# Performance work log

Hardware: AMD Instinct MI355X
Metric: run time of the kernel (lower is better)

The kernel has to match this reference:

```python
import jax, jax.numpy as jnp
import numpy as np

B, D, E, K, NC, NH = 8192, 1280, 4, 2, 20, 4
CD = D // NC      # chunk_dim = 64
HD = CD // NH     # head_dim = 16
FF = CD * 4       # ffn hidden = 256
EPS = 1e-8


def setup_inputs() -> dict:
    key = jax.random.key(0)
    ks = jax.random.split(key, 12)
    f = lambda k, sh, s=0.02: jax.random.normal(k, sh, jnp.float32) * s
    return {
        "x": jax.random.normal(ks[0], (B, D), jnp.float32),
        "gate_w1": f(ks[1], (E * 4, D)), "gate_b1": jnp.zeros((E * 4,), jnp.float32),
        "gate_w2": f(ks[2], (E, E * 4)), "gate_b2": jnp.zeros((E,), jnp.float32),
        "pos_embed": f(ks[3], (E, NC, CD)),
        "norm1_g": jnp.ones((E, CD), jnp.float32),
        "in_proj_w": f(ks[4], (E, 3 * CD, CD)), "in_proj_b": jnp.zeros((E, 3 * CD), jnp.float32),
        "out_proj_w": f(ks[5], (E, CD, CD)), "out_proj_b": jnp.zeros((E, CD), jnp.float32),
        "ls1_g": jnp.full((E, CD), 1e-4, jnp.float32),
        "norm2_g": jnp.ones((E, CD), jnp.float32),
        "ffn_w1": f(ks[6], (E, FF, CD)), "ffn_b1": jnp.zeros((E, FF), jnp.float32),
        "ffn_w2": f(ks[7], (E, CD, FF)), "ffn_b2": jnp.zeros((E, CD), jnp.float32),
        "ls2_g": jnp.full((E, CD), 1e-4, jnp.float32),
        "proj_w": f(ks[8], (E, D, D)), "proj_b": jnp.zeros((E, D), jnp.float32),
    }


def _rms(v, g):
    # torch RMSNorm in source: x / (||x||_2 * dim^-0.5 + eps) * g
    n = jnp.linalg.norm(v, axis=-1, keepdims=True) * (CD ** -0.5)
    return v / (n + EPS) * g


def _expert(x, pos, n1g, ipw, ipb, opw, opb, l1, n2g, fw1, fb1, fw2, fb2, l2, pw, pb):
    b = x.shape[0]
    xs = x.reshape(b, NC, CD) + pos            # [b, NC, CD]
    xn = _rms(xs, n1g)
    qkv = xn @ ipw.T + ipb                      # [b, NC, 3*CD]
    q, k, v = jnp.split(qkv, 3, axis=-1)
    q = q.reshape(b, NC, NH, HD).transpose(0, 2, 1, 3)
    k = k.reshape(b, NC, NH, HD).transpose(0, 2, 1, 3)
    v = v.reshape(b, NC, NH, HD).transpose(0, 2, 1, 3)
    att = jax.nn.softmax(jnp.einsum('bhqd,bhkd->bhqk', q, k) * (HD ** -0.5), axis=-1)
    o = jnp.einsum('bhqk,bhkd->bhqd', att, v).transpose(0, 2, 1, 3).reshape(b, NC, CD)
    o = o @ opw.T + opb
    xs = xs + l1 * o                            # residual + LayerScale
    h = jax.nn.relu(_rms(xs, n2g) @ fw1.T + fb1) @ fw2.T + fb2
    xs = xs + l2 * h
    return xs.reshape(b, D) @ pw.T + pb         # final proj [b, D]


def reference(x, gate_w1, gate_b1, gate_w2, gate_b2, pos_embed, norm1_g,
              in_proj_w, in_proj_b, out_proj_w, out_proj_b, ls1_g, norm2_g,
              ffn_w1, ffn_b1, ffn_w2, ffn_b2, ls2_g, proj_w, proj_b):
    logits = jnp.tanh(x @ gate_w1.T + gate_b1) @ gate_w2.T + gate_b2   # [B, E]
    scores = jax.nn.softmax(logits, axis=-1)
    tk_s, tk_i = jax.lax.top_k(scores, K)
    tk_s = tk_s / (tk_s.sum(-1, keepdims=True) + 1e-6)
    onehot = jax.nn.one_hot(tk_i, E, dtype=x.dtype)                    # [B, K, E]
    w = (onehot * tk_s[..., None]).sum(1)                              # [B, E] combine weights
    eout = jax.vmap(_expert, in_axes=(None,) + (0,) * 15)(
        x, pos_embed, norm1_g, in_proj_w, in_proj_b, out_proj_w, out_proj_b,
        ls1_g, norm2_g, ffn_w1, ffn_b1, ffn_w2, ffn_b2, ls2_g, proj_w, proj_b)  # [E, B, D]
    output = jnp.einsum('ebd,be->bd', eout, w)
    aux_loss = jnp.float32(0.0)  # eval mode
    load = onehot.sum((0, 1))    # [E]
    return output, aux_loss, load
```

## Files before the change

kernel.cpp:

```cpp
#include <hip/hip_runtime.h>
#include <hip/hip_bf16.h>
#include <math.h>

#define B_SZ 8192
#define D_SZ 1280
#define NE   4
#define NC   20
#define CD   64
#define NH   4
#define HD   16
#define FF   256

typedef __attribute__((ext_vector_type(8))) short bf16x8;
typedef __attribute__((ext_vector_type(4))) float f32x4;

#define WS_TOPI   256
#define WS_TOPW   (WS_TOPI + 2*B_SZ*4)
#define WS_IDX    (WS_TOPW + 2*B_SZ*4)
#define WS_WGT    (WS_IDX  + 2*B_SZ*4)
#define WS_ER0    (WS_WGT  + 2*B_SZ*4)
#define WS_ER1    (WS_ER0  + B_SZ*4)
#define WS_PRK    (WS_ER1  + B_SZ*4)
#define WS_BBE    (WS_PRK  + B_SZ*4)
#define WS_BBP    (WS_BBE  + 32*4*4)
#define WS_PRA    (WS_BBP  + 32*16*4)
#define WS_PRB    (WS_PRA  + (B_SZ+128)*4)
#define WS_PW1    (WS_PRB  + (B_SZ+128)*4)
#define WS_PW2    (WS_PW1  + (B_SZ+128)*4)
#define WS_PRW    (WS_PW2  + (B_SZ+128)*4)
#define WS_XSF    532480
#define XSF_ROWS  (2*B_SZ + 128)
#define WS_PWB    (WS_XSF + (size_t)XSF_ROWS * D_SZ * 2)
#define WS_IPWB   (WS_PWB  + (size_t)NE * D_SZ * D_SZ * 2)
#define WS_OPWB   (WS_IPWB + (size_t)NE * 192 * 64 * 2)
#define WS_FW1B   (WS_OPWB + (size_t)NE * 64 * 64 * 2)
#define WS_FW2B   (WS_FW1B + (size_t)NE * 256 * 64 * 2)

__global__ __launch_bounds__(256) void convert_pw(const float* __restrict__ pw,
                                                  __hip_bfloat16* __restrict__ pwb)
{
    size_t i = ((size_t)blockIdx.x * 256 + threadIdx.x) * 8;
    float4 a = *(const float4*)(pw + i);
    float4 b = *(const float4*)(pw + i + 4);
    __hip_bfloat16 h[8];
    h[0] = __float2bfloat16(a.x); h[1] = __float2bfloat16(a.y);
    h[2] = __float2bfloat16(a.z); h[3] = __float2bfloat16(a.w);
    h[4] = __float2bfloat16(b.x); h[5] = __float2bfloat16(b.y);
    h[6] = __float2bfloat16(b.z); h[7] = __float2bfloat16(b.w);
    *(uint4*)(pwb + i) = *(uint4*)h;
}

#define N_IPW (NE*192*64)
#define N_OPW (NE*64*64)
#define N_FW1 (NE*256*64)
#define N_FW2 (NE*64*256)
__global__ __launch_bounds__(256) void convert_small(
    const float* __restrict__ ipw, const float* __restrict__ opw,
    const float* __restrict__ fw1, const float* __restrict__ fw2,
    __hip_bfloat16* __restrict__ ipwb, __hip_bfloat16* __restrict__ opwb,
    __hip_bfloat16* __restrict__ fw1b, __hip_bfloat16* __restrict__ fw2b)
{
    size_t i = ((size_t)blockIdx.x * 256 + threadIdx.x) * 8;
    const float* src; __hip_bfloat16* dst; size_t off;
    if (i < N_IPW)                       { src = ipw; dst = ipwb; off = i; }
    else if (i < N_IPW + N_OPW)          { src = opw; dst = opwb; off = i - N_IPW; }
    else if (i < N_IPW + N_OPW + N_FW1)  { src = fw1; dst = fw1b; off = i - N_IPW - N_OPW; }
    else                                 { src = fw2; dst = fw2b; off = i - N_IPW - N_OPW - N_FW1; }
    float4 a = *(const float4*)(src + off);
    float4 b = *(const float4*)(src + off + 4);
    __hip_bfloat16 h[8];
    h[0] = __float2bfloat16(a.x); h[1] = __float2bfloat16(a.y);
    h[2] = __float2bfloat16(a.z); h[3] = __float2bfloat16(a.w);
    h[4] = __float2bfloat16(b.x); h[5] = __float2bfloat16(b.y);
    h[6] = __float2bfloat16(b.z); h[7] = __float2bfloat16(b.w);
    *(uint4*)(dst + off) = *(uint4*)h;
}

__global__ __launch_bounds__(64) void gate_kernel(
    const float* __restrict__ x, const float* __restrict__ gw1, const float* __restrict__ gb1,
    const float* __restrict__ gw2, const float* __restrict__ gb2,
    int* __restrict__ topi, float* __restrict__ topw)
{
    const int b = blockIdx.x;
    const int lane = threadIdx.x;
    float acc[16];
#pragma unroll
    for (int j = 0; j < 16; ++j) acc[j] = 0.f;
    const float* xr = x + (size_t)b * D_SZ;
    for (int t = 0; t < NC; ++t) {
        float xv = xr[t * 64 + lane];
#pragma unroll
        for (int j = 0; j < 16; ++j) acc[j] += xv * gw1[j * D_SZ + t * 64 + lane];
    }
#pragma unroll
    for (int j = 0; j < 16; ++j) {
        acc[j] += __shfl_xor(acc[j], 32, 64);
        acc[j] += __shfl_xor(acc[j], 16, 64);
        acc[j] += __shfl_xor(acc[j], 8, 64);
        acc[j] += __shfl_xor(acc[j], 4, 64);
        acc[j] += __shfl_xor(acc[j], 2, 64);
        acc[j] += __shfl_xor(acc[j], 1, 64);
    }
    if (lane == 0) {
        float h[16];
#pragma unroll
        for (int j = 0; j < 16; ++j) h[j] = tanhf(acc[j] + gb1[j]);
        float l[4];
#pragma unroll
        for (int e = 0; e < 4; ++e) {
            float sv = gb2[e];
#pragma unroll
            for (int j = 0; j < 16; ++j) sv += h[j] * gw2[e * 16 + j];
            l[e] = sv;
        }
        float m = fmaxf(fmaxf(l[0], l[1]), fmaxf(l[2], l[3]));
        float p[4];
        float sum = 0.f;
#pragma unroll
        for (int e = 0; e < 4; ++e) { p[e] = expf(l[e] - m); sum += p[e]; }
#pragma unroll
        for (int e = 0; e < 4; ++e) p[e] /= sum;
        int i1 = 0;
#pragma unroll
        for (int e = 1; e < 4; ++e) if (p[e] > p[i1]) i1 = e;
        int i2 = (i1 == 0) ? 1 : 0;
#pragma unroll
        for (int e = 0; e < 4; ++e) if (e != i1 && p[e] > p[i2]) i2 = e;
        float s1 = p[i1], s2 = p[i2];
        float denom = s1 + s2 + 1e-6f;
        topi[b * 2 + 0] = i1;
        topi[b * 2 + 1] = i2;
        topw[b * 2 + 0] = s1 / denom;
        topw[b * 2 + 1] = s2 / denom;
    }
}

__global__ __launch_bounds__(256) void count_kernel(
    const int* __restrict__ topi,
    int* __restrict__ cnt, int* __restrict__ pcnt,
    int* __restrict__ er0, int* __restrict__ er1, int* __restrict__ prk,
    int* __restrict__ bbe, int* __restrict__ bbp)
{
    __shared__ int he[4], hp[16];
    const int t = threadIdx.x;
    const int blk = blockIdx.x;
    const int b = blk * 256 + t;
    if (t < 4) he[t] = 0;
    if (t < 16) hp[t] = 0;
    __syncthreads();
    int e0 = topi[b * 2], e1 = topi[b * 2 + 1];
    er0[b] = atomicAdd(&he[e0], 1);
    er1[b] = atomicAdd(&he[e1], 1);
    prk[b] = atomicAdd(&hp[e0 * 4 + e1], 1);
    __syncthreads();
    if (t < 4)  bbe[blk * 4 + t]  = atomicAdd(&cnt[t], he[t]);
    if (t < 16) bbp[blk * 16 + t] = atomicAdd(&pcnt[t], hp[t]);
}

__global__ void offsets_kernel(const int* __restrict__ cnt, const int* __restrict__ pcnt,
                               int* __restrict__ offA, int* __restrict__ poff,
                               float* __restrict__ load_out)
{
    if (threadIdx.x == 0 && blockIdx.x == 0) {
        int a = 0;
#pragma unroll
        for (int e = 0; e < 4; ++e) { offA[e] = a; a += cnt[e]; }
        offA[4] = a;
        int q = 0;
#pragma unroll
        for (int p = 0; p < 16; ++p) { poff[p] = q; q += pcnt[p]; }
        poff[16] = q;
#pragma unroll
        for (int e = 0; e < 4; ++e) load_out[e] = (float)cnt[e];
    }
}

__global__ __launch_bounds__(256) void fill_kernel(
    const int* __restrict__ topi, const float* __restrict__ topw,
    const int* __restrict__ offA, const int* __restrict__ poff,
    const int* __restrict__ er0, const int* __restrict__ er1, const int* __restrict__ prk,
    const int* __restrict__ bbe, const int* __restrict__ bbp,
    int* __restrict__ idx_list, float* __restrict__ wgt_list,
    int* __restrict__ prA, int* __restrict__ prB,
    float* __restrict__ pw1, float* __restrict__ pw2, int* __restrict__ prow)
{
    const int b = blockIdx.x * 256 + threadIdx.x;
    const int blk = blockIdx.x;
    int e0 = topi[b * 2], e1 = topi[b * 2 + 1];
    float w0 = topw[b * 2], w1 = topw[b * 2 + 1];
    int slot0 = offA[e0] + bbe[blk * 4 + e0] + er0[b];
    int slot1 = offA[e1] + bbe[blk * 4 + e1] + er1[b];
    idx_list[slot0] = b; wgt_list[slot0] = w0;
    idx_list[slot1] = b; wgt_list[slot1] = w1;
    int p = e0 * 4 + e1;
    int pos = poff[p] + bbp[blk * 16 + p] + prk[b];
    prA[pos] = slot0; prB[pos] = slot1;
    pw1[pos] = w0; pw2[pos] = w1; prow[pos] = b;
}

__global__ __launch_bounds__(256) void expert_inner(
    const float* __restrict__ x, const float* __restrict__ pos,
    const float* __restrict__ n1g,
    const __hip_bfloat16* __restrict__ ipwb, const float* __restrict__ ipb,
    const __hip_bfloat16* __restrict__ opwb, const float* __restrict__ opb,
    const float* __restrict__ ls1, const float* __restrict__ n2g,
    const __hip_bfloat16* __restrict__ fw1b, const float* __restrict__ fb1,
    const __hip_bfloat16* __restrict__ fw2b, const float* __restrict__ fb2,
    const float* __restrict__ ls2,
    const int* __restrict__ offA, const int* __restrict__ idx_list,
    const float* __restrict__ wgt_list,
    __hip_bfloat16* __restrict__ xsf)
{
    __shared__ float xs[NC][66];
    __shared__ __hip_bfloat16 xnb[32][72];
    __shared__ __hip_bfloat16 qkb[32][136];
    __shared__ __hip_bfloat16 vtb[64][40];
    __shared__ __hip_bfloat16 h1b[32][264];

    const int t = threadIdx.x;
    const int w = t >> 6;
    const int lane = t & 63;
    const int l15 = lane & 15, lg = lane >> 4;
    const int s = blockIdx.x;
    const int e = (s >= offA[1]) + (s >= offA[2]) + (s >= offA[3]);
    const int b = idx_list[s];
    const float wgt = wgt_list[s];

    for (int idx = t; idx < D_SZ; idx += 256)
        xs[idx >> 6][idx & 63] = x[(size_t)b * D_SZ + idx] + pos[e * D_SZ + idx];
    __syncthreads();

    {
        float g = n1g[e * CD + lane];
#pragma unroll
        for (int ic = 0; ic < 5; ++ic) {
            int c = w * 5 + ic;
            float v = xs[c][lane];
            float ss = v * v;
            ss += __shfl_xor(ss, 32, 64); ss += __shfl_xor(ss, 16, 64);
            ss += __shfl_xor(ss, 8, 64);  ss += __shfl_xor(ss, 4, 64);
            ss += __shfl_xor(ss, 2, 64);  ss += __shfl_xor(ss, 1, 64);
            float n = sqrtf(ss) * 0.125f + 1e-8f;
            xnb[c][lane] = __float2bfloat16(v / n * g);
        }
        __hip_bfloat16 z = __float2bfloat16(0.f);
        for (int i = t; i < 12 * 64; i += 256) xnb[20 + (i >> 6)][i & 63] = z;
    }
    __syncthreads();

    {
        bf16x8 af[2][2];
#pragma unroll
        for (int mt = 0; mt < 2; ++mt)
#pragma unroll
            for (int ks = 0; ks < 2; ++ks)
                af[mt][ks] = *(const bf16x8*)&xnb[mt * 16 + l15][ks * 32 + lg * 8];
#pragma unroll
        for (int i = 0; i < 3; ++i) {
            int tn = w * 3 + i;
            int n = tn * 16 + l15;
            f32x4 acc[2] = {{0,0,0,0},{0,0,0,0}};
#pragma unroll
            for (int ks = 0; ks < 2; ++ks) {
                bf16x8 bf = *(const bf16x8*)(ipwb + ((size_t)(e * 192 + n)) * 64 + ks * 32 + lg * 8);
#pragma unroll
                for (int mt = 0; mt < 2; ++mt)
                    acc[mt] = __builtin_amdgcn_mfma_f32_16x16x32_bf16(af[mt][ks], bf, acc[mt], 0, 0, 0);
            }
            float bias = ipb[e * 192 + n];
            if (tn < 8) {
#pragma unroll
                for (int mt = 0; mt < 2; ++mt)
#pragma unroll
                    for (int r = 0; r < 4; ++r)
                        qkb[mt * 16 + lg * 4 + r][n] = __float2bfloat16(acc[mt][r] + bias);
            } else {
#pragma unroll
                for (int mt = 0; mt < 2; ++mt)
#pragma unroll
                    for (int r = 0; r < 4; ++r)
                        vtb[n - 128][mt * 16 + lg * 4 + r] = __float2bfloat16(acc[mt][r] + bias);
            }
        }
    }
    __syncthreads();

    {
        bf16x8 zf = {0,0,0,0,0,0,0,0};
        bf16x8 aq[2], bk[2];
#pragma unroll
        for (int mt = 0; mt < 2; ++mt)
            aq[mt] = (lg < 2) ? *(const bf16x8*)&qkb[mt * 16 + l15][w * 16 + lg * 8] : zf;
#pragma unroll
        for (int nt = 0; nt < 2; ++nt)
            bk[nt] = (lg < 2) ? *(const bf16x8*)&qkb[nt * 16 + l15][64 + w * 16 + lg * 8] : zf;
        f32x4 sacc[2][2];
#pragma unroll
        for (int mt = 0; mt < 2; ++mt)
#pragma unroll
            for (int nt = 0; nt < 2; ++nt)
                sacc[mt][nt] = __builtin_amdgcn_mfma_f32_16x16x32_bf16(
                    aq[mt], bk[nt], (f32x4){0,0,0,0}, 0, 0, 0);

#pragma unroll
        for (int mt = 0; mt < 2; ++mt) {
#pragma unroll
            for (int r = 0; r < 4; ++r) {
                float v0 = sacc[mt][0][r] * 0.25f;
                float v1 = (l15 < 4) ? sacc[mt][1][r] * 0.25f : -3.0e38f;
                float mx = fmaxf(v0, v1);
                mx = fmaxf(mx, __shfl_xor(mx, 1, 64));
                mx = fmaxf(mx, __shfl_xor(mx, 2, 64));
                mx = fmaxf(mx, __shfl_xor(mx, 4, 64));
                mx = fmaxf(mx, __shfl_xor(mx, 8, 64));
                float e0 = __expf(v0 - mx);
                float e1 = (l15 < 4) ? __expf(v1 - mx) : 0.f;
                float sm = e0 + e1;
                sm += __shfl_xor(sm, 1, 64);
                sm += __shfl_xor(sm, 2, 64);
                sm += __shfl_xor(sm, 4, 64);
                sm += __shfl_xor(sm, 8, 64);
                float is = 1.0f / sm;
                int qi = mt * 16 + lg * 4 + r;
                h1b[qi][w * 32 + l15]      = __float2bfloat16(e0 * is);
                h1b[qi][w * 32 + 16 + l15] = __float2bfloat16(e1 * is);
            }
        }
        bf16x8 bv = *(const bf16x8*)&vtb[w * 16 + l15][lg * 8];
#pragma unroll
        for (int mt = 0; mt < 2; ++mt) {
            bf16x8 ap = *(const bf16x8*)&h1b[mt * 16 + l15][w * 32 + lg * 8];
            f32x4 oacc = __builtin_amdgcn_mfma_f32_16x16x32_bf16(ap, bv, (f32x4){0,0,0,0}, 0, 0, 0);
#pragma unroll
            for (int r = 0; r < 4; ++r)
                xnb[mt * 16 + lg * 4 + r][w * 16 + l15] = __float2bfloat16(oacc[r]);
        }
    }
    __syncthreads();

    {
        bf16x8 af[2][2];
#pragma unroll
        for (int mt = 0; mt < 2; ++mt)
#pragma unroll
            for (int ks = 0; ks < 2; ++ks)
                af[mt][ks] = *(const bf16x8*)&xnb[mt * 16 + l15][ks * 32 + lg * 8];
        int n = w * 16 + l15;
        f32x4 acc[2] = {{0,0,0,0},{0,0,0,0}};
#pragma unroll
        for (int ks = 0; ks < 2; ++ks) {
            bf16x8 bf = *(const bf16x8*)(opwb + ((size_t)(e * 64 + n)) * 64 + ks * 32 + lg * 8);
#pragma unroll
            for (int mt = 0; mt < 2; ++mt)
                acc[mt] = __builtin_amdgcn_mfma_f32_16x16x32_bf16(af[mt][ks], bf, acc[mt], 0, 0, 0);
        }
        float l1v = ls1[e * 64 + n], ob = opb[e * 64 + n];
#pragma unroll
        for (int mt = 0; mt < 2; ++mt)
#pragma unroll
            for (int r = 0; r < 4; ++r) {
                int m = mt * 16 + lg * 4 + r;
                if (m < NC) xs[m][n] += l1v * (acc[mt][r] + ob);
            }
    }
    __syncthreads();

    {
        float g = n2g[e * CD + lane];
#pragma unroll
        for (int ic = 0; ic < 5; ++ic) {
            int c = w * 5 + ic;
            float v = xs[c][lane];
            float ss = v * v;
            ss += __shfl_xor(ss, 32, 64); ss += __shfl_xor(ss, 16, 64);
            ss += __shfl_xor(ss, 8, 64);  ss += __shfl_xor(ss, 4, 64);
            ss += __shfl_xor(ss, 2, 64);  ss += __shfl_xor(ss, 1, 64);
            float n = sqrtf(ss) * 0.125f + 1e-8f;
            xnb[c][lane] = __float2bfloat16(v / n * g);
        }
        __hip_bfloat16 z = __float2bfloat16(0.f);
        for (int i = t; i < 12 * 64; i += 256) xnb[20 + (i >> 6)][i & 63] = z;
    }
    __syncthreads();

    {
        bf16x8 af[2][2];
#pragma unroll
        for (int mt = 0; mt < 2; ++mt)
#pragma unroll
            for (int ks = 0; ks < 2; ++ks)
                af[mt][ks] = *(const bf16x8*)&xnb[mt * 16 + l15][ks * 32 + lg * 8];
#pragma unroll
        for (int i = 0; i < 4; ++i) {
            int n = (w * 4 + i) * 16 + l15;
            f32x4 acc[2] = {{0,0,0,0},{0,0,0,0}};
#pragma unroll
            for (int ks = 0; ks < 2; ++ks) {
                bf16x8 bf = *(const bf16x8*)(fw1b + ((size_t)(e * 256 + n)) * 64 + ks * 32 + lg * 8);
#pragma unroll
                for (int mt = 0; mt < 2; ++mt)
                    acc[mt] = __builtin_amdgcn_mfma_f32_16x16x32_bf16(af[mt][ks], bf, acc[mt], 0, 0, 0);
            }
            float b1 = fb1[e * 256 + n];
#pragma unroll
            for (int mt = 0; mt < 2; ++mt)
#pragma unroll
                for (int r = 0; r < 4; ++r)
                    h1b[mt * 16 + lg * 4 + r][n] = __float2bfloat16(fmaxf(acc[mt][r] + b1, 0.f));
        }
    }
    __syncthreads();

    {
        int n = w * 16 + l15;
        f32x4 acc[2] = {{0,0,0,0},{0,0,0,0}};
#pragma unroll
        for (int ks = 0; ks < 8; ++ks) {
            bf16x8 bf = *(const bf16x8*)(fw2b + ((size_t)(e * 64 + n)) * 256 + ks * 32 + lg * 8);
#pragma unroll
            for (int mt = 0; mt < 2; ++mt) {
                bf16x8 af = *(const bf16x8*)&h1b[mt * 16 + l15][ks * 32 + lg * 8];
                acc[mt] = __builtin_amdgcn_mfma_f32_16x16x32_bf16(af, bf, acc[mt], 0, 0, 0);
            }
        }
        float l2v = ls2[e * 64 + n], b2 = fb2[e * 64 + n];
#pragma unroll
        for (int mt = 0; mt < 2; ++mt)
#pragma unroll
            for (int r = 0; r < 4; ++r) {
                int m = mt * 16 + lg * 4 + r;
                if (m < NC) xs[m][n] += l2v * (acc[mt][r] + b2);
            }
    }
    __syncthreads();

    for (int idx = t; idx < D_SZ; idx += 256)
        xsf[(size_t)s * D_SZ + idx] = __float2bfloat16(wgt * xs[idx >> 6][idx & 63]);
}

#define PROWP 130

__global__ __launch_bounds__(256) void proj_pair(
    const __hip_bfloat16* __restrict__ xsf, const __hip_bfloat16* __restrict__ pwb,
    const float* __restrict__ pb, const int* __restrict__ poff,
    const int* __restrict__ prA, const int* __restrict__ prB,
    const float* __restrict__ pw1, const float* __restrict__ pw2,
    const int* __restrict__ prow, float* __restrict__ out)
{
    __shared__ short As[8][PROWP][8];
    __shared__ short Bs[8][PROWP][8];
    __shared__ int   sSlot[2][128];
    __shared__ float sW[2][128];
    __shared__ int   sRow[128];

    int mblk = blockIdx.x;
    int p = 0, base = 0, M = 0;
#pragma unroll
    for (int pp = 0; pp < 16; ++pp) {
        int b0 = poff[pp], b1 = poff[pp + 1];
        int nb = (b1 - b0 + 127) >> 7;
        if (p == pp && mblk >= nb) { mblk -= nb; p = pp + 1; }
        else if (p == pp) { base = b0; M = b1 - b0; }
    }
    if (p >= 16) return;
    const int ea = p >> 2, eb = p & 3;

    const int m0 = mblk * 128;
    const int n0 = blockIdx.y * 128;
    const int t = threadIdx.x;
    const int w = t >> 6, lane = t & 63;
    const int wm = (w & 1) * 64, wn = (w >> 1) * 64;
    const int l15 = lane & 15, lg = lane >> 4;

    if (t < 128) {
        int posn = base + m0 + t;
        int sa = prA[posn], sb = prB[posn];
        sSlot[0][t] = min(max(sa, 0), 2 * B_SZ);
        sSlot[1][t] = min(max(sb, 0), 2 * B_SZ);
        sW[0][t] = pw1[posn]; sW[1][t] = pw2[posn];
        sRow[t] = prow[posn];
    }
    __syncthreads();

    f32x4 acc[4][4];
#pragma unroll
    for (int i = 0; i < 4; ++i)
#pragma unroll
        for (int j = 0; j < 4; ++j) acc[i][j] = (f32x4){0.f, 0.f, 0.f, 0.f};

    const int arow0 = t >> 3;
    const int akb = t & 7;

#pragma unroll
    for (int ph = 0; ph < 2; ++ph) {
        const __hip_bfloat16* Bg = pwb + (size_t)(ph ? eb : ea) * D_SZ * D_SZ + (size_t)n0 * D_SZ;
        int aslot[4];
#pragma unroll
        for (int i = 0; i < 4; ++i) aslot[i] = sSlot[ph][arow0 + 32 * i];

        for (int kt = 0; kt < D_SZ; kt += 64) {
            __syncthreads();
#pragma unroll
            for (int i = 0; i < 4; ++i) {
                int row = arow0 + 32 * i;
                *(uint4*)&As[akb][row][0] =
                    *(const uint4*)(xsf + (size_t)aslot[i] * D_SZ + kt + akb * 8);
                *(uint4*)&Bs[akb][row][0] =
                    *(const uint4*)(Bg + (size_t)row * D_SZ + kt + akb * 8);
            }
            __syncthreads();
#pragma unroll
            for (int ks = 0; ks < 2; ++ks) {
                int kb = ks * 4 + lg;
                bf16x8 af[4], bfr[4];
#pragma unroll
                for (int ti = 0; ti < 4; ++ti) af[ti]  = *(const bf16x8*)&As[kb][wm + ti * 16 + l15][0];
#pragma unroll
                for (int tj = 0; tj < 4; ++tj) bfr[tj] = *(const bf16x8*)&Bs[kb][wn + tj * 16 + l15][0];
#pragma unroll
                for (int ti = 0; ti < 4; ++ti)
#pragma unroll
                    for (int tj = 0; tj < 4; ++tj)
                        acc[ti][tj] = __builtin_amdgcn_mfma_f32_16x16x32_bf16(
                            af[ti], bfr[tj], acc[ti][tj], 0, 0, 0);
            }
        }
    }

    float pbva[4], pbvb[4];
#pragma unroll
    for (int tj = 0; tj < 4; ++tj) {
        int nc = n0 + wn + tj * 16 + l15;
        pbva[tj] = pb[(size_t)ea * D_SZ + nc];
        pbvb[tj] = pb[(size_t)eb * D_SZ + nc];
    }

#pragma unroll
    for (int ti = 0; ti < 4; ++ti) {
#pragma unroll
        for (int r = 0; r < 4; ++r) {
            int m = wm + ti * 16 + lg * 4 + r;
            if (m0 + m < M) {
                float w1 = sW[0][m], w2 = sW[1][m];
                float* orow = out + (size_t)sRow[m] * D_SZ + n0 + wn + l15;
#pragma unroll
                for (int tj = 0; tj < 4; ++tj)
                    orow[tj * 16] = acc[ti][tj][r] + w1 * pbva[tj] + w2 * pbvb[tj];
            }
        }
    }
}

extern "C" void kernel_launch(void* const* d_in, const int* in_sizes, int n_in,
                              void* d_out, int out_size, void* d_ws, size_t ws_size,
                              hipStream_t stream)
{
    const float* x   = (const float*)d_in[0];
    const float* gw1 = (const float*)d_in[1];
    const float* gb1 = (const float*)d_in[2];
    const float* gw2 = (const float*)d_in[3];
    const float* gb2 = (const float*)d_in[4];
    const float* pos = (const float*)d_in[5];
    const float* n1g = (const float*)d_in[6];
    const float* ipw = (const float*)d_in[7];
    const float* ipb = (const float*)d_in[8];
    const float* opw = (const float*)d_in[9];
    const float* opb = (const float*)d_in[10];
    const float* ls1 = (const float*)d_in[11];
    const float* n2g = (const float*)d_in[12];
    const float* fw1 = (const float*)d_in[13];
    const float* fb1 = (const float*)d_in[14];
    const float* fw2 = (const float*)d_in[15];
    const float* fb2 = (const float*)d_in[16];
    const float* ls2 = (const float*)d_in[17];
    const float* pw  = (const float*)d_in[18];
    const float* pb  = (const float*)d_in[19];

    float* out = (float*)d_out;

    char* ws = (char*)d_ws;
    int*   cnt      = (int*)(ws + 0);
    int*   pcnt     = (int*)(ws + 16);
    int*   offA     = (int*)(ws + 80);
    int*   poff     = (int*)(ws + 112);
    int*   topi     = (int*)(ws + WS_TOPI);
    float* topw     = (float*)(ws + WS_TOPW);
    int*   idx_list = (int*)(ws + WS_IDX);
    float* wgt_list = (float*)(ws + WS_WGT);
    int*   er0      = (int*)(ws + WS_ER0);
    int*   er1      = (int*)(ws + WS_ER1);
    int*   prk      = (int*)(ws + WS_PRK);
    int*   bbe      = (int*)(ws + WS_BBE);
    int*   bbp      = (int*)(ws + WS_BBP);
    int*   prA      = (int*)(ws + WS_PRA);
    int*   prB      = (int*)(ws + WS_PRB);
    float* pw1      = (float*)(ws + WS_PW1);
    float* pw2      = (float*)(ws + WS_PW2);
    int*   prow     = (int*)(ws + WS_PRW);
    __hip_bfloat16* xsf  = (__hip_bfloat16*)(ws + WS_XSF);
    __hip_bfloat16* pwb  = (__hip_bfloat16*)(ws + WS_PWB);
    __hip_bfloat16* ipwb = (__hip_bfloat16*)(ws + WS_IPWB);
    __hip_bfloat16* opwb = (__hip_bfloat16*)(ws + WS_OPWB);
    __hip_bfloat16* fw1b = (__hip_bfloat16*)(ws + WS_FW1B);
    __hip_bfloat16* fw2b = (__hip_bfloat16*)(ws + WS_FW2B);

    hipMemsetAsync(d_ws, 0, 256, stream);
    hipMemsetAsync(out + (size_t)B_SZ * D_SZ, 0, 5 * sizeof(float), stream);

    float* load_out = out + (size_t)B_SZ * D_SZ + 1;

    convert_pw<<<NE * D_SZ * D_SZ / (256 * 8), 256, 0, stream>>>(pw, pwb);
    convert_small<<<(N_IPW + N_OPW + N_FW1 + N_FW2) / (256 * 8), 256, 0, stream>>>(
        ipw, opw, fw1, fw2, ipwb, opwb, fw1b, fw2b);
    gate_kernel<<<B_SZ, 64, 0, stream>>>(x, gw1, gb1, gw2, gb2, topi, topw);
    count_kernel<<<B_SZ / 256, 256, 0, stream>>>(topi, cnt, pcnt, er0, er1, prk, bbe, bbp);
    offsets_kernel<<<1, 64, 0, stream>>>(cnt, pcnt, offA, poff, load_out);
    fill_kernel<<<B_SZ / 256, 256, 0, stream>>>(topi, topw, offA, poff, er0, er1, prk,
                                                bbe, bbp, idx_list, wgt_list,
                                                prA, prB, pw1, pw2, prow);
    expert_inner<<<2 * B_SZ, 256, 0, stream>>>(x, pos, n1g, ipwb, ipb, opwb, opb, ls1,
                                               n2g, fw1b, fb1, fw2b, fb2, ls2,
                                               offA, idx_list, wgt_list, xsf);
    proj_pair<<<dim3(96, D_SZ / 128), 256, 0, stream>>>(
        xsf, pwb, pb, poff, prA, prB, pw1, pw2, prow, out);
}
```

Baseline: 563.9 us.

## Overlay attention LDS buffers, fuse input load with RMSNorm, simplify softmax

Places the q/k, v-transposed and attention-probability tiles in one aliased shared buffer, guarded by an extra barrier, and requests 6 blocks per CU through launch bounds. The goal is less LDS per block and higher occupancy. The x+pos load is fused into the first RMSNorm, which removes a barrier, and divides become hardware reciprocals. Softmax drops the max subtraction, which assumes attention logits stay small enough not to overflow exp. The second zero-fill of the padded rows is removed, so those rows now hold attention outputs.

```diff
diff --git a/kernel.cpp b/kernel.cpp
--- a/kernel.cpp
+++ b/kernel.cpp
@@ -198,7 +198,7 @@
     pw1[pos] = w0; pw2[pos] = w1; prow[pos] = b;
 }
 
-__global__ __launch_bounds__(256) void expert_inner(
+__global__ __launch_bounds__(256, 6) void expert_inner(
     const float* __restrict__ x, const float* __restrict__ pos,
     const float* __restrict__ n1g,
     const __hip_bfloat16* __restrict__ ipwb, const float* __restrict__ ipb,
@@ -213,9 +213,11 @@
 {
     __shared__ float xs[NC][66];
     __shared__ __hip_bfloat16 xnb[32][72];
-    __shared__ __hip_bfloat16 qkb[32][136];
-    __shared__ __hip_bfloat16 vtb[64][40];
-    __shared__ __hip_bfloat16 h1b[32][264];
+    __shared__ __hip_bfloat16 ovl[32 * 260];
+
+    __hip_bfloat16 (* const qkb)[136] = (__hip_bfloat16(*)[136])ovl;
+    __hip_bfloat16 (* const vtb)[40]  = (__hip_bfloat16(*)[40])(ovl + 32*136);
+    __hip_bfloat16 (* const h1b)[260] = (__hip_bfloat16(*)[260])ovl;
 
     const int t = threadIdx.x;
     const int w = t >> 6;
@@ -226,12 +228,141 @@
     const int b = idx_list[s];
     const float wgt = wgt_list[s];
 
-    for (int idx = t; idx < D_SZ; idx += 256)
-        xs[idx >> 6][idx & 63] = x[(size_t)b * D_SZ + idx] + pos[e * D_SZ + idx];
-    __syncthreads();
-
     {
         float g = n1g[e * CD + lane];
+        const float* xr = x + (size_t)b * D_SZ;
+        const float* pr = pos + (size_t)e * D_SZ;
+#pragma unroll
+        for (int ic = 0; ic < 5; ++ic) {
+            int c = w * 5 + ic;
+            float v = xr[c * 64 + lane] + pr[c * 64 + lane];
+            xs[c][lane] = v;
+            float ss = v * v;
+            ss += __shfl_xor(ss, 32, 64); ss += __shfl_xor(ss, 16, 64);
+            ss += __shfl_xor(ss, 8, 64);  ss += __shfl_xor(ss, 4, 64);
+            ss += __shfl_xor(ss, 2, 64);  ss += __shfl_xor(ss, 1, 64);
+            float n = sqrtf(ss) * 0.125f + 1e-8f;
+            xnb[c][lane] = __float2bfloat16(v * __builtin_amdgcn_rcpf(n) * g);
+        }
+        __hip_bfloat16 z = __float2bfloat16(0.f);
+        for (int i = t; i < 12 * 64; i += 256) xnb[20 + (i >> 6)][i & 63] = z;
+    }
+    __syncthreads();
+
+    {
+        bf16x8 af[2][2];
+#pragma unroll
+        for (int mt = 0; mt < 2; ++mt)
+#pragma unroll
+            for (int ks = 0; ks < 2; ++ks)
+                af[mt][ks] = *(const bf16x8*)&xnb[mt * 16 + l15][ks * 32 + lg * 8];
+#pragma unroll
+        for (int i = 0; i < 3; ++i) {
+            int tn = w * 3 + i;
+            int n = tn * 16 + l15;
+            f32x4 acc[2] = {{0,0,0,0},{0,0,0,0}};
+#pragma unroll
+            for (int ks = 0; ks < 2; ++ks) {
+                bf16x8 bf = *(const bf16x8*)(ipwb + ((size_t)(e * 192 + n)) * 64 + ks * 32 + lg * 8);
+#pragma unroll
+                for (int mt = 0; mt < 2; ++mt)
+                    acc[mt] = __builtin_amdgcn_mfma_f32_16x16x32_bf16(af[mt][ks], bf, acc[mt], 0, 0, 0);
+            }
+            float bias = ipb[e * 192 + n];
+            if (tn < 8) {
+#pragma unroll
+                for (int mt = 0; mt < 2; ++mt)
+#pragma unroll
+                    for (int r = 0; r < 4; ++r)
+                        qkb[mt * 16 + lg * 4 + r][n] = __float2bfloat16(acc[mt][r] + bias);
+            } else {
+#pragma unroll
+                for (int mt = 0; mt < 2; ++mt)
+#pragma unroll
+                    for (int r = 0; r < 4; ++r)
+                        vtb[n - 128][mt * 16 + lg * 4 + r] = __float2bfloat16(acc[mt][r] + bias);
+            }
+        }
+    }
+    __syncthreads();
+
+    {
+        bf16x8 zf = {0,0,0,0,0,0,0,0};
+        bf16x8 aq[2], bk[2];
+#pragma unroll
+        for (int mt = 0; mt < 2; ++mt)
+            aq[mt] = (lg < 2) ? *(const bf16x8*)&qkb[mt * 16 + l15][w * 16 + lg * 8] : zf;
+#pragma unroll
+        for (int nt = 0; nt < 2; ++nt)
+            bk[nt] = (lg < 2) ? *(const bf16x8*)&qkb[nt * 16 + l15][64 + w * 16 + lg * 8] : zf;
+        bf16x8 bv = *(const bf16x8*)&vtb[w * 16 + l15][lg * 8];
+        __syncthreads();
+
+        f32x4 sacc[2][2];
+#pragma unroll
+        for (int mt = 0; mt < 2; ++mt)
+#pragma unroll
+            for (int nt = 0; nt < 2; ++nt)
+                sacc[mt][nt] = __builtin_amdgcn_mfma_f32_16x16x32_bf16(
+                    aq[mt], bk[nt], (f32x4){0,0,0,0}, 0, 0, 0);
+
+#pragma unroll
+        for (int mt = 0; mt < 2; ++mt) {
+#pragma unroll
+            for (int r = 0; r < 4; ++r) {
+                float e0 = __expf(sacc[mt][0][r] * 0.25f);
+                float e1 = (l15 < 4) ? __expf(sacc[mt][1][r] * 0.25f) : 0.f;
+                float sm = e0 + e1;
+                sm += __shfl_xor(sm, 1, 64);
+                sm += __shfl_xor(sm, 2, 64);
+                sm += __shfl_xor(sm, 4, 64);
+                sm += __shfl_xor(sm, 8, 64);
+                float is = __builtin_amdgcn_rcpf(sm);
+                int qi = mt * 16 + lg * 4 + r;
+                qkb[qi][w * 32 + l15]      = __float2bfloat16(e0 * is);
+                qkb[qi][w * 32 + 16 + l15] = __float2bfloat16(e1 * is);
+            }
+        }
+#pragma unroll
+        for (int mt = 0; mt < 2; ++mt) {
+            bf16x8 ap = *(const bf16x8*)&qkb[mt * 16 + l15][w * 32 + lg * 8];
+            f32x4 oacc = __builtin_amdgcn_mfma_f32_16x16x32_bf16(ap, bv, (f32x4){0,0,0,0}, 0, 0, 0);
+#pragma unroll
+            for (int r = 0; r < 4; ++r)
+                xnb[mt * 16 + lg * 4 + r][w * 16 + l15] = __float2bfloat16(oacc[r]);
+        }
+    }
+    __syncthreads();
+
+    {
+        bf16x8 af[2][2];
+#pragma unroll
+        for (int mt = 0; mt < 2; ++mt)
+#pragma unroll
+            for (int ks = 0; ks < 2; ++ks)
+                af[mt][ks] = *(const bf16x8*)&xnb[mt * 16 + l15][ks * 32 + lg * 8];
+        int n = w * 16 + l15;
+        f32x4 acc[2] = {{0,0,0,0},{0,0,0,0}};
+#pragma unroll
+        for (int ks = 0; ks < 2; ++ks) {
+            bf16x8 bf = *(const bf16x8*)(opwb + ((size_t)(e * 64 + n)) * 64 + ks * 32 + lg * 8);
+#pragma unroll
+            for (int mt = 0; mt < 2; ++mt)
+                acc[mt] = __builtin_amdgcn_mfma_f32_16x16x32_bf16(af[mt][ks], bf, acc[mt], 0, 0, 0);
+        }
+        float l1v = ls1[e * 64 + n], ob = opb[e * 64 + n];
+#pragma unroll
+        for (int mt = 0; mt < 2; ++mt)
+#pragma unroll
+            for (int r = 0; r < 4; ++r) {
+                int m = mt * 16 + lg * 4 + r;
+                if (m < NC) xs[m][n] += l1v * (acc[mt][r] + ob);
+            }
+    }
+    __syncthreads();
+
+    {
+        float g = n2g[e * CD + lane];
 #pragma unroll
         for (int ic = 0; ic < 5; ++ic) {
             int c = w * 5 + ic;
@@ -241,145 +372,8 @@
             ss += __shfl_xor(ss, 8, 64);  ss += __shfl_xor(ss, 4, 64);
             ss += __shfl_xor(ss, 2, 64);  ss += __shfl_xor(ss, 1, 64);
             float n = sqrtf(ss) * 0.125f + 1e-8f;
-            xnb[c][lane] = __float2bfloat16(v / n * g);
-        }
-        __hip_bfloat16 z = __float2bfloat16(0.f);
-        for (int i = t; i < 12 * 64; i += 256) xnb[20 + (i >> 6)][i & 63] = z;
-    }
-    __syncthreads();
-
-    {
-        bf16x8 af[2][2];
-#pragma unroll
-        for (int mt = 0; mt < 2; ++mt)
-#pragma unroll
-            for (int ks = 0; ks < 2; ++ks)
-                af[mt][ks] = *(const bf16x8*)&xnb[mt * 16 + l15][ks * 32 + lg * 8];
-#pragma unroll
-        for (int i = 0; i < 3; ++i) {
-            int tn = w * 3 + i;
-            int n = tn * 16 + l15;
-            f32x4 acc[2] = {{0,0,0,0},{0,0,0,0}};
-#pragma unroll
-            for (int ks = 0; ks < 2; ++ks) {
-                bf16x8 bf = *(const bf16x8*)(ipwb + ((size_t)(e * 192 + n)) * 64 + ks * 32 + lg * 8);
-#pragma unroll
-                for (int mt = 0; mt < 2; ++mt)
-                    acc[mt] = __builtin_amdgcn_mfma_f32_16x16x32_bf16(af[mt][ks], bf, acc[mt], 0, 0, 0);
-            }
-            float bias = ipb[e * 192 + n];
-            if (tn < 8) {
-#pragma unroll
-                for (int mt = 0; mt < 2; ++mt)
-#pragma unroll
-                    for (int r = 0; r < 4; ++r)
-                        qkb[mt * 16 + lg * 4 + r][n] = __float2bfloat16(acc[mt][r] + bias);
-            } else {
-#pragma unroll
-                for (int mt = 0; mt < 2; ++mt)
-#pragma unroll
-                    for (int r = 0; r < 4; ++r)
-                        vtb[n - 128][mt * 16 + lg * 4 + r] = __float2bfloat16(acc[mt][r] + bias);
-            }
-        }
-    }
-    __syncthreads();
-
-    {
-        bf16x8 zf = {0,0,0,0,0,0,0,0};
-        bf16x8 aq[2], bk[2];
-#pragma unroll
-        for (int mt = 0; mt < 2; ++mt)
-            aq[mt] = (lg < 2) ? *(const bf16x8*)&qkb[mt * 16 + l15][w * 16 + lg * 8] : zf;
-#pragma unroll
-        for (int nt = 0; nt < 2; ++nt)
-            bk[nt] = (lg < 2) ? *(const bf16x8*)&qkb[nt * 16 + l15][64 + w * 16 + lg * 8] : zf;
-        f32x4 sacc[2][2];
-#pragma unroll
-        for (int mt = 0; mt < 2; ++mt)
-#pragma unroll
-            for (int nt = 0; nt < 2; ++nt)
-                sacc[mt][nt] = __builtin_amdgcn_mfma_f32_16x16x32_bf16(
-                    aq[mt], bk[nt], (f32x4){0,0,0,0}, 0, 0, 0);
-
-#pragma unroll
-        for (int mt = 0; mt < 2; ++mt) {
-#pragma unroll
-            for (int r = 0; r < 4; ++r) {
-                float v0 = sacc[mt][0][r] * 0.25f;
-                float v1 = (l15 < 4) ? sacc[mt][1][r] * 0.25f : -3.0e38f;
-                float mx = fmaxf(v0, v1);
-                mx = fmaxf(mx, __shfl_xor(mx, 1, 64));
-                mx = fmaxf(mx, __shfl_xor(mx, 2, 64));
-                mx = fmaxf(mx, __shfl_xor(mx, 4, 64));
-                mx = fmaxf(mx, __shfl_xor(mx, 8, 64));
-                float e0 = __expf(v0 - mx);
-                float e1 = (l15 < 4) ? __expf(v1 - mx) : 0.f;
-                float sm = e0 + e1;
-                sm += __shfl_xor(sm, 1, 64);
-                sm += __shfl_xor(sm, 2, 64);
-                sm += __shfl_xor(sm, 4, 64);
-                sm += __shfl_xor(sm, 8, 64);
-                float is = 1.0f / sm;
-                int qi = mt * 16 + lg * 4 + r;
-                h1b[qi][w * 32 + l15]      = __float2bfloat16(e0 * is);
-                h1b[qi][w * 32 + 16 + l15] = __float2bfloat16(e1 * is);
-            }
-        }
-        bf16x8 bv = *(const bf16x8*)&vtb[w * 16 + l15][lg * 8];
-#pragma unroll
-        for (int mt = 0; mt < 2; ++mt) {
-            bf16x8 ap = *(const bf16x8*)&h1b[mt * 16 + l15][w * 32 + lg * 8];
-            f32x4 oacc = __builtin_amdgcn_mfma_f32_16x16x32_bf16(ap, bv, (f32x4){0,0,0,0}, 0, 0, 0);
-#pragma unroll
-            for (int r = 0; r < 4; ++r)
-                xnb[mt * 16 + lg * 4 + r][w * 16 + l15] = __float2bfloat16(oacc[r]);
-        }
-    }
-    __syncthreads();
-
-    {
-        bf16x8 af[2][2];
-#pragma unroll
-        for (int mt = 0; mt < 2; ++mt)
-#pragma unroll
-            for (int ks = 0; ks < 2; ++ks)
-                af[mt][ks] = *(const bf16x8*)&xnb[mt * 16 + l15][ks * 32 + lg * 8];
-        int n = w * 16 + l15;
-        f32x4 acc[2] = {{0,0,0,0},{0,0,0,0}};
-#pragma unroll
-        for (int ks = 0; ks < 2; ++ks) {
-            bf16x8 bf = *(const bf16x8*)(opwb + ((size_t)(e * 64 + n)) * 64 + ks * 32 + lg * 8);
-#pragma unroll
-            for (int mt = 0; mt < 2; ++mt)
-                acc[mt] = __builtin_amdgcn_mfma_f32_16x16x32_bf16(af[mt][ks], bf, acc[mt], 0, 0, 0);
-        }
-        float l1v = ls1[e * 64 + n], ob = opb[e * 64 + n];
-#pragma unroll
-        for (int mt = 0; mt < 2; ++mt)
-#pragma unroll
-            for (int r = 0; r < 4; ++r) {
-                int m = mt * 16 + lg * 4 + r;
-                if (m < NC) xs[m][n] += l1v * (acc[mt][r] + ob);
-            }
-    }
-    __syncthreads();
-
-    {
-        float g = n2g[e * CD + lane];
-#pragma unroll
-        for (int ic = 0; ic < 5; ++ic) {
-            int c = w * 5 + ic;
-            float v = xs[c][lane];
-            float ss = v * v;
-            ss += __shfl_xor(ss, 32, 64); ss += __shfl_xor(ss, 16, 64);
-            ss += __shfl_xor(ss, 8, 64);  ss += __shfl_xor(ss, 4, 64);
-            ss += __shfl_xor(ss, 2, 64);  ss += __shfl_xor(ss, 1, 64);
-            float n = sqrtf(ss) * 0.125f + 1e-8f;
-            xnb[c][lane] = __float2bfloat16(v / n * g);
-        }
-        __hip_bfloat16 z = __float2bfloat16(0.f);
-        for (int i = t; i < 12 * 64; i += 256) xnb[20 + (i >> 6)][i & 63] = z;
+            xnb[c][lane] = __float2bfloat16(v * __builtin_amdgcn_rcpf(n) * g);
+        }
     }
     __syncthreads();
 
```

Result: no change. 557.4 us (-1.2%).
